# Performance work log

Hardware: AMD Instinct MI355X
Metric: run time of the kernel (lower is better)

The kernel has to match this reference:

```python
import jax, jax.numpy as jnp
import numpy as np


def setup_inputs() -> dict:
    key = jax.random.key(0)
    k1, k2 = jax.random.split(key)
    N, K, D = 65536, 512, 512
    x = jax.random.normal(k1, (N, D), dtype=jnp.float32)
    centroids = jax.random.normal(k2, (K, D), dtype=jnp.float32)
    return {"x": x, "centroids": centroids}


def reference(x, centroids):
    # Squared pairwise distances via matmul expansion (same math as
    # sum((x[:,None,:] - c[None,:,:])**2, axis=2), without the [N,K,D] blowup):
    x_sq = jnp.sum(x * x, axis=1, keepdims=True)            # [N, 1]
    c_sq = jnp.sum(centroids * centroids, axis=1)            # [K]
    d2 = x_sq + c_sq[None, :] - 2.0 * (x @ centroids.T)      # [N, K]
    q = 1.0 / (1.0 + d2)                                     # Student-t kernel, alpha=1
    q = q / jnp.sum(q, axis=1, keepdims=True)                # row normalize
    return q
```

## Files before the change

### kernel.cpp

```cpp
#include <hip/hip_runtime.h>
#include <stdint.h>


#define D 512
#define K 512
#define BM 64
#define BK 64
#define NCHUNK (D / BK)
#define THREADS 512

typedef __attribute__((ext_vector_type(8))) short short8;
typedef __attribute__((ext_vector_type(4))) float floatx4;

__device__ __forceinline__ uint16_t f2bf(float f) {
  uint32_t u = __float_as_uint(f);
  u += 0x7FFFu + ((u >> 16) & 1u);
  return (uint16_t)(u >> 16);
}

__global__ __launch_bounds__(64)
void prep_kernel(const float* __restrict__ cent, float* __restrict__ csq,
                 uint16_t* __restrict__ bbf) {
  const int row  = blockIdx.x;
  const int lane = threadIdx.x;
  const float4* src = (const float4*)(cent + (size_t)row * D + lane * 8);
  float4 v0 = src[0];
  float4 v1 = src[1];
  float ss = v0.x*v0.x + v0.y*v0.y + v0.z*v0.z + v0.w*v0.w
           + v1.x*v1.x + v1.y*v1.y + v1.z*v1.z + v1.w*v1.w;
  uint4 pk;
  pk.x = (uint32_t)f2bf(v0.x) | ((uint32_t)f2bf(v0.y) << 16);
  pk.y = (uint32_t)f2bf(v0.z) | ((uint32_t)f2bf(v0.w) << 16);
  pk.z = (uint32_t)f2bf(v1.x) | ((uint32_t)f2bf(v1.y) << 16);
  pk.w = (uint32_t)f2bf(v1.z) | ((uint32_t)f2bf(v1.w) << 16);
  const int c = lane >> 3;
  const int g = lane & 7;
  const int slot = (c * K + row) * 8 + (g ^ (row & 7));
  *(uint4*)(bbf + (size_t)slot * 8) = pk;
  #pragma unroll
  for (int m = 1; m < 64; m <<= 1) ss += __shfl_xor(ss, m);
  if (lane == 0) csq[row] = ss;
}

__global__ __launch_bounds__(THREADS, 4)
void cluster_main(const float* __restrict__ x, const uint16_t* __restrict__ bbf,
                  const float* __restrict__ csq, float* __restrict__ out) {
  __shared__ __align__(16) uint16_t lA[BM * BK];
  __shared__ __align__(16) uint16_t lB[K * BK];
  __shared__ float lcsq[K];
  __shared__ float lxsq[BM];
  __shared__ float lrow[BM];

  const int tid  = threadIdx.x;
  const int wave = tid >> 6;
  const int lane = tid & 63;
  const int p    = lane & 15;
  const int quad = lane >> 4;
  const int row0 = blockIdx.x * BM;

  lcsq[tid] = csq[tid];
  if (tid < BM) { lxsq[tid] = 0.f; lrow[tid] = 0.f; }

  const int ar = tid >> 3;
  const int ag = tid & 7;
  const float* aptr = x + (size_t)(row0 + ar) * D + ag * 8;
  uint16_t* adst = &lA[(size_t)(ar * 8 + (ag ^ (ar & 7))) * 8];
  float xacc = 0.f;

  floatx4 acc[4][4];
  #pragma unroll
  for (int mi = 0; mi < 4; ++mi)
    #pragma unroll
    for (int ni = 0; ni < 4; ++ni)
      acc[mi][ni] = (floatx4){0.f, 0.f, 0.f, 0.f};

  for (int c = 0; c < NCHUNK; ++c) {
    __syncthreads();

    float4 v0 = *(const float4*)(aptr);
    float4 v1 = *(const float4*)(aptr + 4);
    aptr += BK;
    xacc += v0.x*v0.x + v0.y*v0.y + v0.z*v0.z + v0.w*v0.w
          + v1.x*v1.x + v1.y*v1.y + v1.z*v1.z + v1.w*v1.w;
    uint4 pk;
    pk.x = (uint32_t)f2bf(v0.x) | ((uint32_t)f2bf(v0.y) << 16);
    pk.y = (uint32_t)f2bf(v0.z) | ((uint32_t)f2bf(v0.w) << 16);
    pk.z = (uint32_t)f2bf(v1.x) | ((uint32_t)f2bf(v1.y) << 16);
    pk.w = (uint32_t)f2bf(v1.z) | ((uint32_t)f2bf(v1.w) << 16);
    *(uint4*)adst = pk;

    {
      const uint16_t* bsrc = bbf + (size_t)c * (K * BK) + wave * 4096 + lane * 8;
      #pragma unroll
      for (int j = 0; j < 8; ++j) {
        __builtin_amdgcn_global_load_lds(
            (const __attribute__((address_space(1))) uint32_t*)(bsrc + j * 512),
            (__attribute__((address_space(3))) uint32_t*)(&lB[wave * 4096 + j * 512]),
            16, 0, 0);
      }
    }

    __syncthreads();

    #pragma unroll
    for (int kk = 0; kk < 2; ++kk) {
      short8 af[4], bfr[4];
      #pragma unroll
      for (int mi = 0; mi < 4; ++mi) {
        const int r = mi * 16 + p;
        const int g = (kk * 4 + quad) ^ (r & 7);
        af[mi] = *(const short8*)&lA[(size_t)(r * 8 + g) * 8];
      }
      #pragma unroll
      for (int ni = 0; ni < 4; ++ni) {
        const int r = wave * 64 + ni * 16 + p;
        const int g = (kk * 4 + quad) ^ (r & 7);
        bfr[ni] = *(const short8*)&lB[(size_t)(r * 8 + g) * 8];
      }
      #pragma unroll
      for (int mi = 0; mi < 4; ++mi)
        #pragma unroll
        for (int ni = 0; ni < 4; ++ni)
          acc[mi][ni] = __builtin_amdgcn_mfma_f32_16x16x32_bf16(
              af[mi], bfr[ni], acc[mi][ni], 0, 0, 0);
    }
  }

  atomicAdd(&lxsq[ar], xacc);
  __syncthreads();

  float xs[4][4];
  #pragma unroll
  for (int mi = 0; mi < 4; ++mi)
    #pragma unroll
    for (int rr = 0; rr < 4; ++rr)
      xs[mi][rr] = lxsq[mi * 16 + quad * 4 + rr];
  float cs[4];
  #pragma unroll
  for (int ni = 0; ni < 4; ++ni)
    cs[ni] = lcsq[wave * 64 + ni * 16 + p];

  float rp[4][4];
  #pragma unroll
  for (int mi = 0; mi < 4; ++mi)
    #pragma unroll
    for (int rr = 0; rr < 4; ++rr)
      rp[mi][rr] = 0.f;

  #pragma unroll
  for (int mi = 0; mi < 4; ++mi)
    #pragma unroll
    for (int ni = 0; ni < 4; ++ni)
      #pragma unroll
      for (int rr = 0; rr < 4; ++rr) {
        const float d = 1.0f + xs[mi][rr] + cs[ni] - 2.0f * acc[mi][ni][rr];
        const float q = __builtin_amdgcn_rcpf(d);
        acc[mi][ni][rr] = q;
        rp[mi][rr] += q;
      }

  #pragma unroll
  for (int mi = 0; mi < 4; ++mi)
    #pragma unroll
    for (int rr = 0; rr < 4; ++rr) {
      float v = rp[mi][rr];
      v += __shfl_xor(v, 1);
      v += __shfl_xor(v, 2);
      v += __shfl_xor(v, 4);
      v += __shfl_xor(v, 8);
      if (p == 0) atomicAdd(&lrow[mi * 16 + quad * 4 + rr], v);
    }
  __syncthreads();

  #pragma unroll
  for (int mi = 0; mi < 4; ++mi) {
    #pragma unroll
    for (int rr = 0; rr < 4; ++rr) {
      const int row = mi * 16 + quad * 4 + rr;
      const float inv = __builtin_amdgcn_rcpf(lrow[row]);
      float* orow = out + (size_t)(row0 + row) * K + wave * 64 + p;
      #pragma unroll
      for (int ni = 0; ni < 4; ++ni)
        orow[ni * 16] = acc[mi][ni][rr] * inv;
    }
  }
}

extern "C" void kernel_launch(void* const* d_in, const int* in_sizes, int n_in,
                              void* d_out, int out_size, void* d_ws, size_t ws_size,
                              hipStream_t stream) {
  const float* x    = (const float*)d_in[0];
  const float* cent = (const float*)d_in[1];
  float* out = (float*)d_out;

  float*    csq = (float*)d_ws;
  uint16_t* bbf = (uint16_t*)((char*)d_ws + 2048);

  const int N = in_sizes[0] / D;
  prep_kernel<<<K, 64, 0, stream>>>(cent, csq, bbf);
  cluster_main<<<N / BM, THREADS, 0, stream>>>(x, bbf, csq, out);
}
```

Before: 259.7 us.

## Load B fragments directly from global, double-buffer A, stage output through LDS

Centroid bf16 data is re-laid out so each lane reads its MFMA B fragments straight from global memory instead of staging all of B in LDS each chunk. The A tile is double-buffered with register prefetch of the next x chunk, so there is one barrier per chunk instead of two. Output is written through an LDS staging buffer so stores become coalesced float4 rows, and the x-norm reduction switches from an LDS atomic to shuffles. The cost is higher global/L2 traffic for B per block, since every block now reads all 512 KB of centroids, plus extra barriers in the epilogue.

```diff
diff --git a/kernel.cpp b/kernel.cpp
--- a/kernel.cpp
+++ b/kernel.cpp
@@ -8,6 +8,7 @@
 #define BK 64
 #define NCHUNK (D / BK)
 #define THREADS 512
+#define ESTRIDE 516
 
 typedef __attribute__((ext_vector_type(8))) short short8;
 typedef __attribute__((ext_vector_type(4))) float floatx4;
@@ -16,6 +17,20 @@
   uint32_t u = __float_as_uint(f);
   u += 0x7FFFu + ((u >> 16) & 1u);
   return (uint16_t)(u >> 16);
+}
+
+__device__ __forceinline__ uint4 pack8(float4 v0, float4 v1) {
+  uint4 pk;
+  pk.x = (uint32_t)f2bf(v0.x) | ((uint32_t)f2bf(v0.y) << 16);
+  pk.y = (uint32_t)f2bf(v0.z) | ((uint32_t)f2bf(v0.w) << 16);
+  pk.z = (uint32_t)f2bf(v1.x) | ((uint32_t)f2bf(v1.y) << 16);
+  pk.w = (uint32_t)f2bf(v1.z) | ((uint32_t)f2bf(v1.w) << 16);
+  return pk;
+}
+
+__device__ __forceinline__ float sq8(float4 v0, float4 v1) {
+  return v0.x*v0.x + v0.y*v0.y + v0.z*v0.z + v0.w*v0.w
+       + v1.x*v1.x + v1.y*v1.y + v1.z*v1.z + v1.w*v1.w;
 }
 
 __global__ __launch_bounds__(64)
@@ -26,16 +41,11 @@
   const float4* src = (const float4*)(cent + (size_t)row * D + lane * 8);
   float4 v0 = src[0];
   float4 v1 = src[1];
-  float ss = v0.x*v0.x + v0.y*v0.y + v0.z*v0.z + v0.w*v0.w
-           + v1.x*v1.x + v1.y*v1.y + v1.z*v1.z + v1.w*v1.w;
-  uint4 pk;
-  pk.x = (uint32_t)f2bf(v0.x) | ((uint32_t)f2bf(v0.y) << 16);
-  pk.y = (uint32_t)f2bf(v0.z) | ((uint32_t)f2bf(v0.w) << 16);
-  pk.z = (uint32_t)f2bf(v1.x) | ((uint32_t)f2bf(v1.y) << 16);
-  pk.w = (uint32_t)f2bf(v1.z) | ((uint32_t)f2bf(v1.w) << 16);
+  float ss = sq8(v0, v1);
+  uint4 pk = pack8(v0, v1);
   const int c = lane >> 3;
   const int g = lane & 7;
-  const int slot = (c * K + row) * 8 + (g ^ (row & 7));
+  const int slot = ((c * 2 + (g >> 2)) * 512 + row) * 4 + (g & 3);
   *(uint4*)(bbf + (size_t)slot * 8) = pk;
   #pragma unroll
   for (int m = 1; m < 64; m <<= 1) ss += __shfl_xor(ss, m);
@@ -45,11 +55,11 @@
 __global__ __launch_bounds__(THREADS, 4)
 void cluster_main(const float* __restrict__ x, const uint16_t* __restrict__ bbf,
                   const float* __restrict__ csq, float* __restrict__ out) {
-  __shared__ __align__(16) uint16_t lA[BM * BK];
-  __shared__ __align__(16) uint16_t lB[K * BK];
-  __shared__ float lcsq[K];
+  __shared__ __align__(16) char smem[32 * ESTRIDE * 4];
   __shared__ float lxsq[BM];
   __shared__ float lrow[BM];
+  uint16_t* const lA = (uint16_t*)smem;
+  float* const ebuf  = (float*)smem;
 
   const int tid  = threadIdx.x;
   const int wave = tid >> 6;
@@ -58,15 +68,16 @@
   const int quad = lane >> 4;
   const int row0 = blockIdx.x * BM;
 
-  lcsq[tid] = csq[tid];
-  if (tid < BM) { lxsq[tid] = 0.f; lrow[tid] = 0.f; }
+  if (tid < BM) lrow[tid] = 0.f;
 
   const int ar = tid >> 3;
   const int ag = tid & 7;
-  const float* aptr = x + (size_t)(row0 + ar) * D + ag * 8;
-  uint16_t* adst = &lA[(size_t)(ar * 8 + (ag ^ (ar & 7))) * 8];
+  const int adst = (ar * 8 + (ag ^ (ar & 7))) * 8;
+  const float* xp = x + (size_t)(row0 + ar) * D + ag * 8;
   float xacc = 0.f;
 
+  const uint16_t* const bl = bbf + ((wave * 64 + p) * 32 + quad * 8);
+
   floatx4 acc[4][4];
   #pragma unroll
   for (int mi = 0; mi < 4; ++mi)
@@ -74,59 +85,76 @@
     for (int ni = 0; ni < 4; ++ni)
       acc[mi][ni] = (floatx4){0.f, 0.f, 0.f, 0.f};
 
+  {
+    float4 pv0 = *(const float4*)xp;
+    float4 pv1 = *(const float4*)(xp + 4);
+    xp += BK;
+    xacc += sq8(pv0, pv1);
+    *(uint4*)(lA + adst) = pack8(pv0, pv1);
+  }
+  float4 nv0 = *(const float4*)xp;
+  float4 nv1 = *(const float4*)(xp + 4);
+  xp += BK;
+  asm volatile("s_waitcnt lgkmcnt(0)" ::: "memory");
+  __builtin_amdgcn_s_barrier();
+  asm volatile("" ::: "memory");
+
+  #pragma unroll
   for (int c = 0; c < NCHUNK; ++c) {
-    __syncthreads();
-
-    float4 v0 = *(const float4*)(aptr);
-    float4 v1 = *(const float4*)(aptr + 4);
-    aptr += BK;
-    xacc += v0.x*v0.x + v0.y*v0.y + v0.z*v0.z + v0.w*v0.w
-          + v1.x*v1.x + v1.y*v1.y + v1.z*v1.z + v1.w*v1.w;
-    uint4 pk;
-    pk.x = (uint32_t)f2bf(v0.x) | ((uint32_t)f2bf(v0.y) << 16);
-    pk.y = (uint32_t)f2bf(v0.z) | ((uint32_t)f2bf(v0.w) << 16);
-    pk.z = (uint32_t)f2bf(v1.x) | ((uint32_t)f2bf(v1.y) << 16);
-    pk.w = (uint32_t)f2bf(v1.z) | ((uint32_t)f2bf(v1.w) << 16);
-    *(uint4*)adst = pk;
-
-    {
-      const uint16_t* bsrc = bbf + (size_t)c * (K * BK) + wave * 4096 + lane * 8;
-      #pragma unroll
-      for (int j = 0; j < 8; ++j) {
-        __builtin_amdgcn_global_load_lds(
-            (const __attribute__((address_space(1))) uint32_t*)(bsrc + j * 512),
-            (__attribute__((address_space(3))) uint32_t*)(&lB[wave * 4096 + j * 512]),
-            16, 0, 0);
-      }
-    }
-
-    __syncthreads();
-
-    #pragma unroll
-    for (int kk = 0; kk < 2; ++kk) {
-      short8 af[4], bfr[4];
-      #pragma unroll
-      for (int mi = 0; mi < 4; ++mi) {
-        const int r = mi * 16 + p;
-        const int g = (kk * 4 + quad) ^ (r & 7);
-        af[mi] = *(const short8*)&lA[(size_t)(r * 8 + g) * 8];
-      }
-      #pragma unroll
-      for (int ni = 0; ni < 4; ++ni) {
-        const int r = wave * 64 + ni * 16 + p;
-        const int g = (kk * 4 + quad) ^ (r & 7);
-        bfr[ni] = *(const short8*)&lB[(size_t)(r * 8 + g) * 8];
-      }
-      #pragma unroll
-      for (int mi = 0; mi < 4; ++mi)
-        #pragma unroll
-        for (int ni = 0; ni < 4; ++ni)
-          acc[mi][ni] = __builtin_amdgcn_mfma_f32_16x16x32_bf16(
-              af[mi], bfr[ni], acc[mi][ni], 0, 0, 0);
+    const uint16_t* const Acur = lA + (c & 1) * (BM * BK);
+    uint16_t* const Anxt = (uint16_t*)lA + ((c & 1) ^ 1) * (BM * BK);
+    const uint16_t* const bc = bl + c * 32768;
+
+    short8 b0[4];
+    #pragma unroll
+    for (int ni = 0; ni < 4; ++ni)
+      b0[ni] = *(const short8*)(bc + ni * 512);
+
+    if (c < NCHUNK - 1) {
+      xacc += sq8(nv0, nv1);
+      *(uint4*)(Anxt + adst) = pack8(nv0, nv1);
+    }
+
+    short8 b1[4];
+    #pragma unroll
+    for (int ni = 0; ni < 4; ++ni)
+      b1[ni] = *(const short8*)(bc + 16384 + ni * 512);
+    if (c < NCHUNK - 2) {
+      nv0 = *(const float4*)xp;
+      nv1 = *(const float4*)(xp + 4);
+      xp += BK;
+    }
+
+    #pragma unroll
+    for (int mi = 0; mi < 4; ++mi) {
+      const int r = mi * 16 + p;
+      short8 af = *(const short8*)(Acur + (r * 8 + (quad ^ (r & 7))) * 8);
+      #pragma unroll
+      for (int ni = 0; ni < 4; ++ni)
+        acc[mi][ni] = __builtin_amdgcn_mfma_f32_16x16x32_bf16(
+            af, b0[ni], acc[mi][ni], 0, 0, 0);
+    }
+    #pragma unroll
+    for (int mi = 0; mi < 4; ++mi) {
+      const int r = mi * 16 + p;
+      short8 af = *(const short8*)(Acur + (r * 8 + ((4 + quad) ^ (r & 7))) * 8);
+      #pragma unroll
+      for (int ni = 0; ni < 4; ++ni)
+        acc[mi][ni] = __builtin_amdgcn_mfma_f32_16x16x32_bf16(
+            af, b1[ni], acc[mi][ni], 0, 0, 0);
+    }
+
+    if (c < NCHUNK - 1) {
+      asm volatile("s_waitcnt lgkmcnt(0)" ::: "memory");
+      __builtin_amdgcn_s_barrier();
+      asm volatile("" ::: "memory");
     }
   }
 
-  atomicAdd(&lxsq[ar], xacc);
+  xacc += __shfl_xor(xacc, 1);
+  xacc += __shfl_xor(xacc, 2);
+  xacc += __shfl_xor(xacc, 4);
+  if (ag == 0) lxsq[ar] = xacc;
   __syncthreads();
 
   float xs[4][4];
@@ -138,7 +166,7 @@
   float cs[4];
   #pragma unroll
   for (int ni = 0; ni < 4; ++ni)
-    cs[ni] = lcsq[wave * 64 + ni * 16 + p];
+    cs[ni] = csq[wave * 64 + ni * 16 + p];
 
   float rp[4][4];
   #pragma unroll
@@ -172,16 +200,34 @@
     }
   __syncthreads();
 
-  #pragma unroll
-  for (int mi = 0; mi < 4; ++mi) {
-    #pragma unroll
-    for (int rr = 0; rr < 4; ++rr) {
-      const int row = mi * 16 + quad * 4 + rr;
-      const float inv = __builtin_amdgcn_rcpf(lrow[row]);
-      float* orow = out + (size_t)(row0 + row) * K + wave * 64 + p;
+  float inv[4][4];
+  #pragma unroll
+  for (int mi = 0; mi < 4; ++mi)
+    #pragma unroll
+    for (int rr = 0; rr < 4; ++rr)
+      inv[mi][rr] = __builtin_amdgcn_rcpf(lrow[mi * 16 + quad * 4 + rr]);
+
+  #pragma unroll
+  for (int pass = 0; pass < 2; ++pass) {
+    if (pass) __syncthreads();
+    #pragma unroll
+    for (int h = 0; h < 2; ++h) {
+      const int mi = pass * 2 + h;
       #pragma unroll
       for (int ni = 0; ni < 4; ++ni)
-        orow[ni * 16] = acc[mi][ni][rr] * inv;
+        #pragma unroll
+        for (int rr = 0; rr < 4; ++rr)
+          ebuf[(h * 16 + quad * 4 + rr) * ESTRIDE + wave * 64 + ni * 16 + p] =
+              acc[mi][ni][rr] * inv[mi][rr];
+    }
+    __syncthreads();
+    #pragma unroll
+    for (int j = 0; j < 8; ++j) {
+      const int idx = j * 512 + tid;
+      const int r  = idx >> 7;
+      const int c4 = idx & 127;
+      const float4 v = *(const float4*)&ebuf[r * ESTRIDE + c4 * 4];
+      *(float4*)(out + (size_t)(row0 + pass * 32 + r) * K + c4 * 4) = v;
     }
   }
 }
```

New measurement: 257.1 us. Within noise of the previous version (-1.0%).
